# Performance work log

Measured on AMD Instinct MI355X. Metric: run time of the kernel, lower is better.

The kernel has to match this reference:

```python
import jax, jax.numpy as jnp
import numpy as np

jax.config.update("jax_enable_x64", True)  # 64-bit hashes for collision-free WL signatures

N_NODES = 100_000
N_FEATURES = 64
N_EDGES = 6_400_000
NUM_ITERATIONS = 3
STEP = 1


def setup_inputs() -> dict:
    key = jax.random.key(0)
    kx, ke = jax.random.split(key)
    x = jax.random.normal(kx, (N_NODES, N_FEATURES), dtype=jnp.float32)  # one-hot-ish label scores
    edge_index = jax.random.randint(ke, (2, N_EDGES), 0, N_NODES, dtype=jnp.int64)
    return {"x": x, "edge_index": edge_index}


def _splitmix64(z):
    # High-quality 64-bit mixer (uint64, wraps mod 2^64).
    z = z + jnp.uint64(0x9E3779B97F4A7C15)
    z = (z ^ (z >> jnp.uint64(30))) * jnp.uint64(0xBF58476D1CE4E5B9)
    z = (z ^ (z >> jnp.uint64(27))) * jnp.uint64(0x94D049BB133111EB)
    return z ^ (z >> jnp.uint64(31))


def _wl_conv(colors, src, dst, offset):
    """One WL refinement: hash (own color, multiset of neighbor colors), then
    relabel signatures by first-occurrence order (matches PyG WLConv's dict
    insertion order), continuing the global color counter `offset` (matches the
    persistent hashmap across iterations)."""
    n = colors.shape[0]
    h = _splitmix64(colors.astype(jnp.uint64) + jnp.uint64(1))
    # multiset of neighbor colors -> order-invariant sum of neighbor hashes
    nb_sum = jnp.zeros(n, dtype=jnp.uint64).at[dst].add(h[src])  # [N]
    sig = _splitmix64(h * jnp.uint64(0x100000001B3) + nb_sum)    # [N] signatures
    # first-occurrence relabeling (stable, deterministic)
    _, inv = jnp.unique(sig, size=n, fill_value=jnp.uint64(0), return_inverse=True)
    idx = jnp.arange(n, dtype=jnp.int64)
    first_idx = jax.ops.segment_min(idx, inv, num_segments=n)  # empty segments -> int64 max
    order = jnp.argsort(first_idx)                              # real uniques come first
    ranks = jnp.zeros(n, dtype=jnp.int64).at[order].set(idx)
    new_colors = offset + ranks[inv]
    num_new = jnp.sum(first_idx < n).astype(jnp.int64)
    return new_colors, offset + num_new


def reference(x, edge_index):
    src, dst = edge_index[0], edge_index[1]
    colors = jnp.argmax(x, axis=1).astype(jnp.int64)  # [N]
    feats = [colors]
    offset = jnp.int64(0)
    for _ in range(NUM_ITERATIONS):
        for _ in range(STEP):
            colors, offset = _wl_conv(colors, src, dst, offset)
        feats.append(colors)
    return jnp.stack(feats, axis=-1)  # [N, NUM_ITERATIONS+1], int64
```

## Files before the change

kernel.cpp:

```cpp
#include <hip/hip_runtime.h>

typedef unsigned long long u64;
typedef unsigned int u32;
typedef unsigned char u8;
typedef int  v4i __attribute__((ext_vector_type(4)));
typedef unsigned int v4u __attribute__((ext_vector_type(4)));

#define TBL_BITS 18
#define TBL_SIZE (1u << TBL_BITS)
#define TBL_MASK (TBL_SIZE - 1u)
#define EMPTY_KEY 0xFFFFFFFFFFFFFFFFull

#define BK_BITS 9
#define BK_SZ   512
#define MAXNB   256
#define PBLK    2048
#define LDSE    3200
#define NSUB    8
#define GSTR    16

__device__ __forceinline__ u64 splitmix64(u64 z) {
    z = z + 0x9E3779B97F4A7C15ull;
    z = (z ^ (z >> 30)) * 0xBF58476D1CE4E5B9ull;
    z = (z ^ (z >> 27)) * 0x94D049BB133111EBull;
    return z ^ (z >> 31);
}

__device__ __forceinline__ v4i nt_load4(const int* p) {
    return __builtin_nontemporal_load((const v4i*)p);
}
__device__ __forceinline__ v4u nt_loadu4(const u32* p) {
    return __builtin_nontemporal_load((const v4u*)p);
}

__global__ __launch_bounds__(256) void partition_argmax(const float* __restrict__ x,
                                                        const int* __restrict__ src,
                                                        const int* __restrict__ dst,
                                                        u32* __restrict__ gcur,
                                                        u32* __restrict__ packed,
                                                        u64* __restrict__ h,
                                                        int* __restrict__ out,
                                                        int n, int mI4, int nbuck, int cap, int per) {
    int t = threadIdx.x, b = blockIdx.x;
    {
        int wv = (b * 256 + t) >> 6, lane = t & 63;
        const int WPG = (PBLK * 256) >> 6;
        for (int row = wv; row < n; row += WPG) {
            float v = x[(size_t)row * 64 + lane];
            int idx = lane;
            #pragma unroll
            for (int off = 32; off >= 1; off >>= 1) {
                float ov = __shfl_xor(v, off);
                int   oi = __shfl_xor(idx, off);
                if (ov > v || (ov == v && oi < idx)) { v = ov; idx = oi; }
            }
            if (lane == 0) {
                h[row] = splitmix64((u64)idx + 1ull);
                out[(size_t)row * 4 + 0] = idx;
            }
        }
    }
    __shared__ u32 pk[LDSE];
    __shared__ u32 spk[LDSE];
    __shared__ u8  bd[LDSE];
    __shared__ u8  sbd[LDSE];
    __shared__ u32 hist[256], adjB[256], cur[256];
    __shared__ u32 wsum[4];
    hist[t] = 0u;
    __syncthreads();
    int i0 = b * per;
    int i1 = i0 + per; if (i1 > mI4) i1 = mI4;
    int nI = i1 - i0; if (nI < 0) nI = 0;
    int nE = nI * 4;
    for (int i = t; i < nI; i += 256) {
        v4i dv = nt_load4(dst + 4 * (size_t)(i0 + i));
        v4i sv = nt_load4(src + 4 * (size_t)(i0 + i));
        u32 d, s, bid;
        d = (u32)dv.x; s = (u32)sv.x; bid = d >> BK_BITS;
        pk[4*i+0] = (s << BK_BITS) | (d & (BK_SZ-1u)); bd[4*i+0] = (u8)bid; atomicAdd(&hist[bid], 1u);
        d = (u32)dv.y; s = (u32)sv.y; bid = d >> BK_BITS;
        pk[4*i+1] = (s << BK_BITS) | (d & (BK_SZ-1u)); bd[4*i+1] = (u8)bid; atomicAdd(&hist[bid], 1u);
        d = (u32)dv.z; s = (u32)sv.z; bid = d >> BK_BITS;
        pk[4*i+2] = (s << BK_BITS) | (d & (BK_SZ-1u)); bd[4*i+2] = (u8)bid; atomicAdd(&hist[bid], 1u);
        d = (u32)dv.w; s = (u32)sv.w; bid = d >> BK_BITS;
        pk[4*i+3] = (s << BK_BITS) | (d & (BK_SZ-1u)); bd[4*i+3] = (u8)bid; atomicAdd(&hist[bid], 1u);
    }
    __syncthreads();
    u32 v = hist[t];
    int lane = t & 63, w = t >> 6;
    int x2 = (int)v;
    #pragma unroll
    for (int o = 1; o < 64; o <<= 1) {
        int y = __shfl_up(x2, o);
        if (lane >= o) x2 += y;
    }
    if (lane == 63) wsum[w] = (u32)x2;
    __syncthreads();
    u32 woff = 0;
    for (int ww = 0; ww < w; ++ww) woff += wsum[ww];
    u32 excl = woff + (u32)x2 - v;
    cur[t] = excl;
    if (t < nbuck && v > 0u) {
        u32 bpos = atomicAdd(&gcur[t * GSTR], v);
        if (bpos > (u32)cap - v) bpos = (u32)cap - v;
        adjB[t] = (u32)t * (u32)cap + bpos - excl;
    }
    __syncthreads();
    for (int i = t; i < nE; i += 256) {
        u32 bb = (u32)bd[i];
        u32 p = atomicAdd(&cur[bb], 1u);
        spk[p] = pk[i];
        sbd[p] = (u8)bb;
    }
    __syncthreads();
    for (int p = t; p < nE; p += 256) {
        packed[adjB[sbd[p]] + (u32)p] = spk[p];
    }
}

__global__ __launch_bounds__(256) void nb_kernel(const u32* __restrict__ packed,
                                                 const u32* __restrict__ gcur,
                                                 const u64* __restrict__ h,
                                                 u64* __restrict__ nb8, size_t nstride,
                                                 u64* __restrict__ keys,
                                                 u32* __restrict__ vals, int nbuck, int cap) {
    int b = blockIdx.x, t = threadIdx.x;
    if (b >= nbuck * NSUB) {
        int base = (b - nbuck * NSUB) * 1024;
        for (int k = t; k < 1024; k += 256) { keys[base + k] = EMPTY_KEY; vals[base + k] = 0xFFFFFFFFu; }
        return;
    }
    int bucket = b >> 3, sub = b & 7;
    __shared__ u64 acc[BK_SZ];
    acc[t] = 0ull; acc[t + 256] = 0ull;
    __syncthreads();
    u32 lo = (u32)bucket * (u32)cap;
    u32 len = gcur[bucket * GSTR];
    u32 q0 = ((len * (u32)sub) >> 3) & ~3u;
    u32 q1 = (sub == 7) ? len : (((len * (u32)(sub + 1)) >> 3) & ~3u);
    u32 nv4 = (q1 - q0) >> 2;
    const u32* pbase = packed + lo + q0;
    for (u32 i = (u32)t; i < nv4; i += 256) {
        v4u vv = nt_loadu4(pbase + 4 * (size_t)i);
        atomicAdd(&acc[vv.x & (BK_SZ - 1u)], h[vv.x >> BK_BITS]);
        atomicAdd(&acc[vv.y & (BK_SZ - 1u)], h[vv.y >> BK_BITS]);
        atomicAdd(&acc[vv.z & (BK_SZ - 1u)], h[vv.z >> BK_BITS]);
        atomicAdd(&acc[vv.w & (BK_SZ - 1u)], h[vv.w >> BK_BITS]);
    }
    for (u32 e = q0 + nv4 * 4 + (u32)t; e < q1; e += 256) {
        u32 vv = packed[lo + e];
        atomicAdd(&acc[vv & (BK_SZ - 1u)], h[vv >> BK_BITS]);
    }
    __syncthreads();
    u64* dstp = nb8 + (size_t)sub * nstride + ((size_t)bucket << BK_BITS);
    dstp[t] = acc[t];
    dstp[t + 256] = acc[t + 256];
}

__global__ void sig_kernel8(const u64* __restrict__ h, const u64* __restrict__ nb8,
                            size_t nstride, u32* __restrict__ slotarr,
                            u64* __restrict__ keys, u32* __restrict__ vals, int n) {
    int i = blockIdx.x * blockDim.x + threadIdx.x;
    if (i >= n) return;
    u64 nbv = 0;
    #pragma unroll
    for (int s = 0; s < NSUB; ++s) nbv += nb8[(size_t)s * nstride + i];
    u64 sg = splitmix64(h[i] * 0x100000001B3ull + nbv);
    u32 slot = (u32)sg & TBL_MASK;
    while (true) {
        u64 k = keys[slot];
        if (k == sg) break;
        if (k == EMPTY_KEY) {
            u64 prev = atomicCAS(&keys[slot], (u64)EMPTY_KEY, sg);
            if (prev == EMPTY_KEY || prev == sg) break;
        }
        slot = (slot + 1u) & TBL_MASK;
    }
    atomicMin(&vals[slot], (u32)i);
    slotarr[i] = slot;
}

__global__ void sig_kernel1(const u64* __restrict__ h, const u64* __restrict__ nb,
                            u32* __restrict__ slotarr, u64* __restrict__ keys,
                            u32* __restrict__ vals, int n) {
    int i = blockIdx.x * blockDim.x + threadIdx.x;
    if (i >= n) return;
    u64 sg = splitmix64(h[i] * 0x100000001B3ull + nb[i]);
    u32 slot = (u32)sg & TBL_MASK;
    while (true) {
        u64 k = keys[slot];
        if (k == sg) break;
        if (k == EMPTY_KEY) {
            u64 prev = atomicCAS(&keys[slot], (u64)EMPTY_KEY, sg);
            if (prev == EMPTY_KEY || prev == sg) break;
        }
        slot = (slot + 1u) & TBL_MASK;
    }
    atomicMin(&vals[slot], (u32)i);
    slotarr[i] = slot;
}

__global__ void count_rank(const u32* __restrict__ slotarr, const u32* __restrict__ vals,
                           u32* __restrict__ f, u32* __restrict__ lrank,
                           u32* __restrict__ partials, int n) {
    int b = blockIdx.x, t = threadIdx.x;
    int i = b * 256 + t;
    u32 isf = 0, fi = 0;
    if (i < n) {
        fi = vals[slotarr[i]];
        f[i] = fi;
        isf = (fi == (u32)i) ? 1u : 0u;
    }
    __shared__ u32 wsum[4];
    u32 lane = t & 63, wv = (u32)t >> 6;
    int x = (int)isf;
    #pragma unroll
    for (int o = 1; o < 64; o <<= 1) {
        int y = __shfl_up(x, o);
        if (lane >= (u32)o) x += y;
    }
    if (lane == 63) wsum[wv] = (u32)x;
    __syncthreads();
    u32 woff = 0;
    for (u32 w = 0; w < wv; ++w) woff += wsum[w];
    if (i < n) lrank[i] = woff + (u32)x - isf;
    if (t == 255) partials[b] = woff + (u32)x;
}

__global__ __launch_bounds__(512) void relabel_fused(const u32* __restrict__ f,
                                                     const u32* __restrict__ lrank,
                                                     const u32* __restrict__ partials,
                                                     u32* __restrict__ offsets, int iter,
                                                     u64* __restrict__ h, int* __restrict__ out,
                                                     int n, int npb) {
    __shared__ u32 pp[512];
    __shared__ u32 ws[8];
    int t = threadIdx.x;
    u32 v = (t < npb) ? partials[t] : 0u;
    int lane = t & 63, w = t >> 6;
    int x = (int)v;
    #pragma unroll
    for (int o = 1; o < 64; o <<= 1) {
        int y = __shfl_up(x, o);
        if (lane >= o) x += y;
    }
    if (lane == 63) ws[w] = (u32)x;
    __syncthreads();
    u32 woff = 0;
    for (int ww = 0; ww < w; ++ww) woff += ws[ww];
    u32 incl = woff + (u32)x;
    pp[t] = incl - v;
    if (blockIdx.x == 0 && t == 511) offsets[iter + 1] = offsets[iter] + incl;
    __syncthreads();
    int i = blockIdx.x * 512 + t;
    if (i >= n) return;
    u32 j = f[i];
    u32 c = offsets[iter] + pp[j >> 8] + lrank[j];
    h[i] = splitmix64((u64)c + 1ull);
    out[(size_t)i * 4 + (iter + 1)] = (int)c;
}


__global__ void argmax_kernel(const float* __restrict__ x, u64* __restrict__ h,
                              int* __restrict__ out, u32* __restrict__ offsets, int n) {
    if (blockIdx.x == 0 && threadIdx.x == 0) offsets[0] = 0u;
    int wave = (int)((blockIdx.x * (u32)blockDim.x + threadIdx.x) >> 6);
    int lane = threadIdx.x & 63;
    if (wave >= n) return;
    float v = x[(size_t)wave * 64 + lane];
    int idx = lane;
    #pragma unroll
    for (int off = 32; off >= 1; off >>= 1) {
        float ov = __shfl_xor(v, off);
        int   oi = __shfl_xor(idx, off);
        if (ov > v || (ov == v && oi < idx)) { v = ov; idx = oi; }
    }
    if (lane == 0) {
        h[wave] = splitmix64((u64)idx + 1ull);
        out[(size_t)wave * 4 + 0] = idx;
    }
}

__global__ void init_iter_kernel(u64* __restrict__ keys, u32* __restrict__ vals,
                                 u64* __restrict__ nb, int n) {
    int i = blockIdx.x * blockDim.x + threadIdx.x;
    if (i < (int)TBL_SIZE) { keys[i] = EMPTY_KEY; vals[i] = 0xFFFFFFFFu; }
    if (i < n) nb[i] = 0ull;
}

__global__ void edge_kernel(const int* __restrict__ src, const int* __restrict__ dst,
                            const u64* __restrict__ h, u64* __restrict__ nb, int m) {
    int stride = gridDim.x * blockDim.x;
    for (int e = blockIdx.x * blockDim.x + threadIdx.x; e < m; e += stride) {
        atomicAdd(&nb[(u32)dst[e]], h[(u32)src[e]]);
    }
}

extern "C" void kernel_launch(void* const* d_in, const int* in_sizes, int n_in,
                              void* d_out, int out_size, void* d_ws, size_t ws_size,
                              hipStream_t stream) {
    const float* x = (const float*)d_in[0];
    const int* ei = (const int*)d_in[1];
    int n = in_sizes[0] / 64;
    int m = in_sizes[1] / 2;
    const int* src = ei;
    const int* dst = ei + m;
    int* out = (int*)d_out;

    const int NPB = (n + 255) / 256;
    const int NRB = (n + 511) / 512;
    const int nbuck = (n + BK_SZ - 1) >> BK_BITS;
    const size_t nstride = (size_t)nbuck << BK_BITS;
    const int mI4 = m >> 2;
    const int per = (mI4 + PBLK - 1) / PBLK;
    const int cap = (int)((((size_t)m / (size_t)(nbuck > 0 ? nbuck : 1)) * 9 / 8 + 2048 + 255) & ~(size_t)255);

    auto align = [](size_t v) { return (v + 255) & ~(size_t)255; };
    const size_t meta_bytes = ((size_t)(MAXNB * GSTR) + 16) * 4;
    size_t sz_meta   = align(meta_bytes);
    size_t sz_packed = align((size_t)nbuck * (size_t)cap * 4);
    size_t sz_h      = align((size_t)n * 8);
    size_t sz_nbp    = align(nstride * 8 * NSUB);
    size_t sz_tblk   = align((size_t)TBL_SIZE * 8);
    size_t sz_tblv   = align((size_t)TBL_SIZE * 4);
    size_t sz_n4     = align((size_t)n * 4);
    size_t sz_small  = align((size_t)512 * 4);
    size_t need_fast = sz_meta + sz_packed + sz_h + sz_nbp + sz_tblk + sz_tblv
                     + 3 * sz_n4 + sz_small + 256;

    char* p = (char*)d_ws;
    bool fast = (ws_size >= need_fast) && (nbuck <= MAXNB) && ((m & 3) == 0)
              && (NPB <= 512) && (per * 4 <= LDSE) && (n >= 256);
    if (fast) {
        u32* meta    = (u32*)p; p += sz_meta;
        u32* gcur    = meta;
        u32* offsets = meta + MAXNB * GSTR;
        u32* packed  = (u32*)p; p += sz_packed;
        u64* h       = (u64*)p; p += sz_h;
        u64* nbp     = (u64*)p; p += sz_nbp;
        u64* keys    = (u64*)p; p += sz_tblk;
        u32* vals    = (u32*)p; p += sz_tblv;
        u32* slotarr = (u32*)p; p += sz_n4;
        u32* f       = (u32*)p; p += sz_n4;
        u32* lrank   = (u32*)p; p += sz_n4;
        u32* partials= (u32*)p;

        hipMemsetAsync(d_ws, 0, meta_bytes, stream);
        partition_argmax<<<PBLK, 256, 0, stream>>>(x, src, dst, gcur, packed, h, out,
                                                   n, mI4, nbuck, cap, per);
        for (int it = 0; it < 3; ++it) {
            nb_kernel    <<<nbuck * NSUB + 256, 256, 0, stream>>>(packed, gcur, h,
                                                                  nbp, nstride, keys, vals, nbuck, cap);
            sig_kernel8  <<<NPB, 256, 0, stream>>>(h, nbp, nstride, slotarr, keys, vals, n);
            count_rank   <<<NPB, 256, 0, stream>>>(slotarr, vals, f, lrank, partials, n);
            relabel_fused<<<NRB, 512, 0, stream>>>(f, lrank, partials, offsets, it, h, out, n, NPB);
        }
    } else {
        u64* h       = (u64*)p; p += sz_h;
        u64* nb      = (u64*)p; p += sz_h;
        u64* keys    = (u64*)p; p += sz_tblk;
        u32* vals    = (u32*)p; p += sz_tblv;
        u32* slotarr = (u32*)p; p += sz_n4;
        u32* f       = (u32*)p; p += sz_n4;
        u32* lrank   = (u32*)p; p += sz_n4;
        u32* partials= (u32*)p; p += sz_small;
        u32* offsets = (u32*)p;

        argmax_kernel<<<(n + 3) / 4, 256, 0, stream>>>(x, h, out, offsets, n);
        for (int it = 0; it < 3; ++it) {
            init_iter_kernel<<<(TBL_SIZE + 255) / 256, 256, 0, stream>>>(keys, vals, nb, n);
            edge_kernel  <<<4096, 256, 0, stream>>>(src, dst, h, nb, m);
            sig_kernel1  <<<NPB, 256, 0, stream>>>(h, nb, slotarr, keys, vals, n);
            count_rank   <<<NPB, 256, 0, stream>>>(slotarr, vals, f, lrank, partials, n);
            relabel_fused<<<NRB, 512, 0, stream>>>(f, lrank, partials, offsets, it, h, out, n, NPB);
        }
    }
}
```

Baseline: 266.1 us.

## Fuse signature hashing into neighbor-sum kernel via last-block completion counter

The neighbor-sum kernel now uses a per-bucket done counter so that the last sub-block finishing a bucket reduces the partial sums and performs the signature hash-table insertion, which removes the separate sig kernel launch. Hash table clearing moves into the argmax kernel for the first iteration and into relabel_fused for later ones. Argmax is split out of the partition kernel into its own launch. NSUB drops from 8 to 4, which halves the partial-sum traffic but leaves fewer blocks per bucket and less parallelism for the edge accumulation. The insertion step now runs only in the last block per bucket, so that tail work is more serialized.

```diff
diff --git a/kernel.cpp b/kernel.cpp
--- a/kernel.cpp
+++ b/kernel.cpp
@@ -16,7 +16,7 @@
 #define MAXNB   256
 #define PBLK    2048
 #define LDSE    3200
-#define NSUB    8
+#define NSUB    4
 #define GSTR    16
 
 __device__ __forceinline__ u64 splitmix64(u64 z) {
@@ -33,39 +33,41 @@
     return __builtin_nontemporal_load((const v4u*)p);
 }
 
-__global__ __launch_bounds__(256) void partition_argmax(const float* __restrict__ x,
-                                                        const int* __restrict__ src,
+__global__ void argmax_init(const float* __restrict__ x, u64* __restrict__ h,
+                            int* __restrict__ out, u64* __restrict__ keys,
+                            u32* __restrict__ vals, int n) {
+    int gid = blockIdx.x * 256 + threadIdx.x;
+    int step = gridDim.x * 256;
+    for (int s = gid; s < (int)TBL_SIZE; s += step) { keys[s] = EMPTY_KEY; vals[s] = 0xFFFFFFFFu; }
+    int wave = gid >> 6;
+    int lane = threadIdx.x & 63;
+    if (wave >= n) return;
+    float v = x[(size_t)wave * 64 + lane];
+    int idx = lane;
+    #pragma unroll
+    for (int off = 32; off >= 1; off >>= 1) {
+        float ov = __shfl_xor(v, off);
+        int   oi = __shfl_xor(idx, off);
+        if (ov > v || (ov == v && oi < idx)) { v = ov; idx = oi; }
+    }
+    if (lane == 0) {
+        h[wave] = splitmix64((u64)idx + 1ull);
+        out[(size_t)wave * 4 + 0] = idx;
+    }
+}
+
+__global__ __launch_bounds__(256) void partition_kernel(const int* __restrict__ src,
                                                         const int* __restrict__ dst,
                                                         u32* __restrict__ gcur,
                                                         u32* __restrict__ packed,
-                                                        u64* __restrict__ h,
-                                                        int* __restrict__ out,
-                                                        int n, int mI4, int nbuck, int cap, int per) {
-    int t = threadIdx.x, b = blockIdx.x;
-    {
-        int wv = (b * 256 + t) >> 6, lane = t & 63;
-        const int WPG = (PBLK * 256) >> 6;
-        for (int row = wv; row < n; row += WPG) {
-            float v = x[(size_t)row * 64 + lane];
-            int idx = lane;
-            #pragma unroll
-            for (int off = 32; off >= 1; off >>= 1) {
-                float ov = __shfl_xor(v, off);
-                int   oi = __shfl_xor(idx, off);
-                if (ov > v || (ov == v && oi < idx)) { v = ov; idx = oi; }
-            }
-            if (lane == 0) {
-                h[row] = splitmix64((u64)idx + 1ull);
-                out[(size_t)row * 4 + 0] = idx;
-            }
-        }
-    }
+                                                        int mI4, int nbuck, int cap, int per) {
     __shared__ u32 pk[LDSE];
     __shared__ u32 spk[LDSE];
     __shared__ u8  bd[LDSE];
     __shared__ u8  sbd[LDSE];
     __shared__ u32 hist[256], adjB[256], cur[256];
     __shared__ u32 wsum[4];
+    int t = threadIdx.x, b = blockIdx.x;
     hist[t] = 0u;
     __syncthreads();
     int i0 = b * per;
@@ -118,26 +120,24 @@
     }
 }
 
-__global__ __launch_bounds__(256) void nb_kernel(const u32* __restrict__ packed,
-                                                 const u32* __restrict__ gcur,
-                                                 const u64* __restrict__ h,
-                                                 u64* __restrict__ nb8, size_t nstride,
-                                                 u64* __restrict__ keys,
-                                                 u32* __restrict__ vals, int nbuck, int cap) {
+__global__ __launch_bounds__(256) void nbsig_kernel(const u32* __restrict__ packed,
+                                                    const u32* __restrict__ gcur,
+                                                    u32* __restrict__ done,
+                                                    const u64* __restrict__ h,
+                                                    u64* __restrict__ nbp, size_t nstride,
+                                                    u64* __restrict__ keys, u32* __restrict__ vals,
+                                                    u32* __restrict__ slotarr,
+                                                    int nbuck, int cap, int n, int it) {
     int b = blockIdx.x, t = threadIdx.x;
-    if (b >= nbuck * NSUB) {
-        int base = (b - nbuck * NSUB) * 1024;
-        for (int k = t; k < 1024; k += 256) { keys[base + k] = EMPTY_KEY; vals[base + k] = 0xFFFFFFFFu; }
-        return;
-    }
-    int bucket = b >> 3, sub = b & 7;
+    int bucket = b >> 2, sub = b & 3;
     __shared__ u64 acc[BK_SZ];
+    __shared__ u32 lastFlag;
     acc[t] = 0ull; acc[t + 256] = 0ull;
     __syncthreads();
     u32 lo = (u32)bucket * (u32)cap;
     u32 len = gcur[bucket * GSTR];
-    u32 q0 = ((len * (u32)sub) >> 3) & ~3u;
-    u32 q1 = (sub == 7) ? len : (((len * (u32)(sub + 1)) >> 3) & ~3u);
+    u32 q0 = ((len * (u32)sub) >> 2) & ~3u;
+    u32 q1 = (sub == NSUB - 1) ? len : (((len * (u32)(sub + 1)) >> 2) & ~3u);
     u32 nv4 = (q1 - q0) >> 2;
     const u32* pbase = packed + lo + q0;
     for (u32 i = (u32)t; i < nv4; i += 256) {
@@ -152,32 +152,150 @@
         atomicAdd(&acc[vv & (BK_SZ - 1u)], h[vv >> BK_BITS]);
     }
     __syncthreads();
-    u64* dstp = nb8 + (size_t)sub * nstride + ((size_t)bucket << BK_BITS);
-    dstp[t] = acc[t];
-    dstp[t + 256] = acc[t + 256];
-}
-
-__global__ void sig_kernel8(const u64* __restrict__ h, const u64* __restrict__ nb8,
-                            size_t nstride, u32* __restrict__ slotarr,
-                            u64* __restrict__ keys, u32* __restrict__ vals, int n) {
+    u64* dp = nbp + (size_t)sub * nstride + ((size_t)bucket << BK_BITS);
+    dp[t] = acc[t];
+    dp[t + 256] = acc[t + 256];
+    __threadfence();
+    __syncthreads();
+    if (t == 0) {
+        u32 old = atomicAdd(&done[bucket * GSTR], 1u);
+        lastFlag = (old == (u32)(it * NSUB + NSUB - 1)) ? 1u : 0u;
+    }
+    __syncthreads();
+    if (!lastFlag) return;
+    __threadfence();
+    u64 s0 = 0, s1 = 0;
+    #pragma unroll
+    for (int s = 0; s < NSUB; ++s) {
+        const u64* pp = nbp + (size_t)s * nstride + ((size_t)bucket << BK_BITS);
+        s0 += pp[t];
+        s1 += pp[t + 256];
+    }
+    int i0 = (bucket << BK_BITS) + t;
+    #pragma unroll
+    for (int half = 0; half < 2; ++half) {
+        int i = i0 + half * 256;
+        u64 nbv = half ? s1 : s0;
+        if (i < n) {
+            u64 sg = splitmix64(h[i] * 0x100000001B3ull + nbv);
+            u32 slot = (u32)sg & TBL_MASK;
+            while (true) {
+                u64 k = keys[slot];
+                if (k == sg) break;
+                if (k == EMPTY_KEY) {
+                    u64 prev = atomicCAS(&keys[slot], (u64)EMPTY_KEY, sg);
+                    if (prev == EMPTY_KEY || prev == sg) break;
+                }
+                slot = (slot + 1u) & TBL_MASK;
+            }
+            atomicMin(&vals[slot], (u32)i);
+            slotarr[i] = slot;
+        }
+    }
+}
+
+__global__ void count_rank(const u32* __restrict__ slotarr, const u32* __restrict__ vals,
+                           u32* __restrict__ f, u32* __restrict__ lrank,
+                           u32* __restrict__ partials, int n) {
+    int b = blockIdx.x, t = threadIdx.x;
+    int i = b * 256 + t;
+    u32 isf = 0, fi = 0;
+    if (i < n) {
+        fi = vals[slotarr[i]];
+        f[i] = fi;
+        isf = (fi == (u32)i) ? 1u : 0u;
+    }
+    __shared__ u32 wsum[4];
+    u32 lane = t & 63, wv = (u32)t >> 6;
+    int x = (int)isf;
+    #pragma unroll
+    for (int o = 1; o < 64; o <<= 1) {
+        int y = __shfl_up(x, o);
+        if (lane >= (u32)o) x += y;
+    }
+    if (lane == 63) wsum[wv] = (u32)x;
+    __syncthreads();
+    u32 woff = 0;
+    for (u32 w = 0; w < wv; ++w) woff += wsum[w];
+    if (i < n) lrank[i] = woff + (u32)x - isf;
+    if (t == 255) partials[b] = woff + (u32)x;
+}
+
+__global__ __launch_bounds__(512) void relabel_fused(const u32* __restrict__ f,
+                                                     const u32* __restrict__ lrank,
+                                                     const u32* __restrict__ partials,
+                                                     u32* __restrict__ offsets, int iter,
+                                                     u64* __restrict__ h, int* __restrict__ out,
+                                                     u64* __restrict__ keys, u32* __restrict__ vals,
+                                                     int clearTbl, int n, int npb) {
+    if (clearTbl) {
+        int step = gridDim.x * 512;
+        for (int s = blockIdx.x * 512 + threadIdx.x; s < (int)TBL_SIZE; s += step) {
+            keys[s] = EMPTY_KEY;
+            vals[s] = 0xFFFFFFFFu;
+        }
+    }
+    __shared__ u32 pp[512];
+    __shared__ u32 ws[8];
+    int t = threadIdx.x;
+    u32 v = (t < npb) ? partials[t] : 0u;
+    int lane = t & 63, w = t >> 6;
+    int x = (int)v;
+    #pragma unroll
+    for (int o = 1; o < 64; o <<= 1) {
+        int y = __shfl_up(x, o);
+        if (lane >= o) x += y;
+    }
+    if (lane == 63) ws[w] = (u32)x;
+    __syncthreads();
+    u32 woff = 0;
+    for (int ww = 0; ww < w; ++ww) woff += ws[ww];
+    u32 incl = woff + (u32)x;
+    pp[t] = incl - v;
+    if (blockIdx.x == 0 && t == 511) offsets[iter + 1] = offsets[iter] + incl;
+    __syncthreads();
+    int i = blockIdx.x * 512 + t;
+    if (i >= n) return;
+    u32 j = f[i];
+    u32 c = offsets[iter] + pp[j >> 8] + lrank[j];
+    h[i] = splitmix64((u64)c + 1ull);
+    out[(size_t)i * 4 + (iter + 1)] = (int)c;
+}
+
+
+__global__ void argmax_kernel(const float* __restrict__ x, u64* __restrict__ h,
+                              int* __restrict__ out, u32* __restrict__ offsets, int n) {
+    if (blockIdx.x == 0 && threadIdx.x == 0) offsets[0] = 0u;
+    int wave = (int)((blockIdx.x * (u32)blockDim.x + threadIdx.x) >> 6);
+    int lane = threadIdx.x & 63;
+    if (wave >= n) return;
+    float v = x[(size_t)wave * 64 + lane];
+    int idx = lane;
+    #pragma unroll
+    for (int off = 32; off >= 1; off >>= 1) {
+        float ov = __shfl_xor(v, off);
+        int   oi = __shfl_xor(idx, off);
+        if (ov > v || (ov == v && oi < idx)) { v = ov; idx = oi; }
+    }
+    if (lane == 0) {
+        h[wave] = splitmix64((u64)idx + 1ull);
+        out[(size_t)wave * 4 + 0] = idx;
+    }
+}
+
+__global__ void init_iter_kernel(u64* __restrict__ keys, u32* __restrict__ vals,
+                                 u64* __restrict__ nb, int n) {
     int i = blockIdx.x * blockDim.x + threadIdx.x;
-    if (i >= n) return;
-    u64 nbv = 0;
-    #pragma unroll
-    for (int s = 0; s < NSUB; ++s) nbv += nb8[(size_t)s * nstride + i];
-    u64 sg = splitmix64(h[i] * 0x100000001B3ull + nbv);
-    u32 slot = (u32)sg & TBL_MASK;
-    while (true) {
-        u64 k = keys[slot];
-        if (k == sg) break;
-        if (k == EMPTY_KEY) {
-            u64 prev = atomicCAS(&keys[slot], (u64)EMPTY_KEY, sg);
-            if (prev == EMPTY_KEY || prev == sg) break;
-        }
-        slot = (slot + 1u) & TBL_MASK;
-    }
-    atomicMin(&vals[slot], (u32)i);
-    slotarr[i] = slot;
+    if (i < (int)TBL_SIZE) { keys[i] = EMPTY_KEY; vals[i] = 0xFFFFFFFFu; }
+    if (i < n) nb[i] = 0ull;
+}
+
+__global__ void edge_kernel(const int* __restrict__ src, const int* __restrict__ dst,
+                            const u64* __restrict__ h, u64* __restrict__ nb, int m) {
+    int stride = gridDim.x * blockDim.x;
+    for (int e = blockIdx.x * blockDim.x + threadIdx.x; e < m; e += stride) {
+        atomicAdd(&nb[(u32)dst[e]], h[(u32)src[e]]);
+    }
 }
 
 __global__ void sig_kernel1(const u64* __restrict__ h, const u64* __restrict__ nb,
@@ -200,102 +318,6 @@
     slotarr[i] = slot;
 }
 
-__global__ void count_rank(const u32* __restrict__ slotarr, const u32* __restrict__ vals,
-                           u32* __restrict__ f, u32* __restrict__ lrank,
-                           u32* __restrict__ partials, int n) {
-    int b = blockIdx.x, t = threadIdx.x;
-    int i = b * 256 + t;
-    u32 isf = 0, fi = 0;
-    if (i < n) {
-        fi = vals[slotarr[i]];
-        f[i] = fi;
-        isf = (fi == (u32)i) ? 1u : 0u;
-    }
-    __shared__ u32 wsum[4];
-    u32 lane = t & 63, wv = (u32)t >> 6;
-    int x = (int)isf;
-    #pragma unroll
-    for (int o = 1; o < 64; o <<= 1) {
-        int y = __shfl_up(x, o);
-        if (lane >= (u32)o) x += y;
-    }
-    if (lane == 63) wsum[wv] = (u32)x;
-    __syncthreads();
-    u32 woff = 0;
-    for (u32 w = 0; w < wv; ++w) woff += wsum[w];
-    if (i < n) lrank[i] = woff + (u32)x - isf;
-    if (t == 255) partials[b] = woff + (u32)x;
-}
-
-__global__ __launch_bounds__(512) void relabel_fused(const u32* __restrict__ f,
-                                                     const u32* __restrict__ lrank,
-                                                     const u32* __restrict__ partials,
-                                                     u32* __restrict__ offsets, int iter,
-                                                     u64* __restrict__ h, int* __restrict__ out,
-                                                     int n, int npb) {
-    __shared__ u32 pp[512];
-    __shared__ u32 ws[8];
-    int t = threadIdx.x;
-    u32 v = (t < npb) ? partials[t] : 0u;
-    int lane = t & 63, w = t >> 6;
-    int x = (int)v;
-    #pragma unroll
-    for (int o = 1; o < 64; o <<= 1) {
-        int y = __shfl_up(x, o);
-        if (lane >= o) x += y;
-    }
-    if (lane == 63) ws[w] = (u32)x;
-    __syncthreads();
-    u32 woff = 0;
-    for (int ww = 0; ww < w; ++ww) woff += ws[ww];
-    u32 incl = woff + (u32)x;
-    pp[t] = incl - v;
-    if (blockIdx.x == 0 && t == 511) offsets[iter + 1] = offsets[iter] + incl;
-    __syncthreads();
-    int i = blockIdx.x * 512 + t;
-    if (i >= n) return;
-    u32 j = f[i];
-    u32 c = offsets[iter] + pp[j >> 8] + lrank[j];
-    h[i] = splitmix64((u64)c + 1ull);
-    out[(size_t)i * 4 + (iter + 1)] = (int)c;
-}
-
-
-__global__ void argmax_kernel(const float* __restrict__ x, u64* __restrict__ h,
-                              int* __restrict__ out, u32* __restrict__ offsets, int n) {
-    if (blockIdx.x == 0 && threadIdx.x == 0) offsets[0] = 0u;
-    int wave = (int)((blockIdx.x * (u32)blockDim.x + threadIdx.x) >> 6);
-    int lane = threadIdx.x & 63;
-    if (wave >= n) return;
-    float v = x[(size_t)wave * 64 + lane];
-    int idx = lane;
-    #pragma unroll
-    for (int off = 32; off >= 1; off >>= 1) {
-        float ov = __shfl_xor(v, off);
-        int   oi = __shfl_xor(idx, off);
-        if (ov > v || (ov == v && oi < idx)) { v = ov; idx = oi; }
-    }
-    if (lane == 0) {
-        h[wave] = splitmix64((u64)idx + 1ull);
-        out[(size_t)wave * 4 + 0] = idx;
-    }
-}
-
-__global__ void init_iter_kernel(u64* __restrict__ keys, u32* __restrict__ vals,
-                                 u64* __restrict__ nb, int n) {
-    int i = blockIdx.x * blockDim.x + threadIdx.x;
-    if (i < (int)TBL_SIZE) { keys[i] = EMPTY_KEY; vals[i] = 0xFFFFFFFFu; }
-    if (i < n) nb[i] = 0ull;
-}
-
-__global__ void edge_kernel(const int* __restrict__ src, const int* __restrict__ dst,
-                            const u64* __restrict__ h, u64* __restrict__ nb, int m) {
-    int stride = gridDim.x * blockDim.x;
-    for (int e = blockIdx.x * blockDim.x + threadIdx.x; e < m; e += stride) {
-        atomicAdd(&nb[(u32)dst[e]], h[(u32)src[e]]);
-    }
-}
-
 extern "C" void kernel_launch(void* const* d_in, const int* in_sizes, int n_in,
                               void* d_out, int out_size, void* d_ws, size_t ws_size,
                               hipStream_t stream) {
@@ -316,7 +338,7 @@
     const int cap = (int)((((size_t)m / (size_t)(nbuck > 0 ? nbuck : 1)) * 9 / 8 + 2048 + 255) & ~(size_t)255);
 
     auto align = [](size_t v) { return (v + 255) & ~(size_t)255; };
-    const size_t meta_bytes = ((size_t)(MAXNB * GSTR) + 16) * 4;
+    const size_t meta_bytes = ((size_t)(2 * MAXNB * GSTR) + 16) * 4;
     size_t sz_meta   = align(meta_bytes);
     size_t sz_packed = align((size_t)nbuck * (size_t)cap * 4);
     size_t sz_h      = align((size_t)n * 8);
@@ -334,7 +356,8 @@
     if (fast) {
         u32* meta    = (u32*)p; p += sz_meta;
         u32* gcur    = meta;
-        u32* offsets = meta + MAXNB * GSTR;
+        u32* done    = meta + MAXNB * GSTR;
+        u32* offsets = meta + 2 * MAXNB * GSTR;
         u32* packed  = (u32*)p; p += sz_packed;
         u64* h       = (u64*)p; p += sz_h;
         u64* nbp     = (u64*)p; p += sz_nbp;
@@ -346,14 +369,15 @@
         u32* partials= (u32*)p;
 
         hipMemsetAsync(d_ws, 0, meta_bytes, stream);
-        partition_argmax<<<PBLK, 256, 0, stream>>>(x, src, dst, gcur, packed, h, out,
-                                                   n, mI4, nbuck, cap, per);
+        argmax_init<<<(n + 3) / 4, 256, 0, stream>>>(x, h, out, keys, vals, n);
+        partition_kernel<<<PBLK, 256, 0, stream>>>(src, dst, gcur, packed, mI4, nbuck, cap, per);
+
         for (int it = 0; it < 3; ++it) {
-            nb_kernel    <<<nbuck * NSUB + 256, 256, 0, stream>>>(packed, gcur, h,
-                                                                  nbp, nstride, keys, vals, nbuck, cap);
-            sig_kernel8  <<<NPB, 256, 0, stream>>>(h, nbp, nstride, slotarr, keys, vals, n);
+            nbsig_kernel <<<nbuck * NSUB, 256, 0, stream>>>(packed, gcur, done, h, nbp, nstride,
+                                                            keys, vals, slotarr, nbuck, cap, n, it);
             count_rank   <<<NPB, 256, 0, stream>>>(slotarr, vals, f, lrank, partials, n);
-            relabel_fused<<<NRB, 512, 0, stream>>>(f, lrank, partials, offsets, it, h, out, n, NPB);
+            relabel_fused<<<NRB, 512, 0, stream>>>(f, lrank, partials, offsets, it, h, out,
+                                                   keys, vals, (it < 2) ? 1 : 0, n, NPB);
         }
     } else {
         u64* h       = (u64*)p; p += sz_h;
@@ -372,7 +396,8 @@
             edge_kernel  <<<4096, 256, 0, stream>>>(src, dst, h, nb, m);
             sig_kernel1  <<<NPB, 256, 0, stream>>>(h, nb, slotarr, keys, vals, n);
             count_rank   <<<NPB, 256, 0, stream>>>(slotarr, vals, f, lrank, partials, n);
-            relabel_fused<<<NRB, 512, 0, stream>>>(f, lrank, partials, offsets, it, h, out, n, NPB);
+            relabel_fused<<<NRB, 512, 0, stream>>>(f, lrank, partials, offsets, it, h, out,
+                                                   keys, vals, 0, n, NPB);
         }
     }
 }
```

After: 598.4 us. 125% more time.
